# Performance work log

Measured on AMD Instinct MI355X. Metric: run time of the kernel, lower is better.

## Reference

```python
import jax, jax.numpy as jnp
import numpy as np

LN_EPS = 1e-5

def setup_inputs() -> dict:
    key = jax.random.key(0)
    ks = jax.random.split(key, 8)
    B, d, var_dim, hidden = 1024, 32, 64, 256
    in_dim = d * var_dim
    causal_vars = jax.random.normal(ks[0], (B, d, var_dim), dtype=jnp.float32)
    adj_soft = jax.random.uniform(ks[1], (d, d), dtype=jnp.float32)
    # Per-variable MLP params (stacked along leading d axis), torch-default-like init scale
    s1 = 1.0 / np.sqrt(in_dim)
    s2 = 1.0 / np.sqrt(hidden)
    W1 = jax.random.uniform(ks[2], (d, in_dim, hidden), minval=-s1, maxval=s1, dtype=jnp.float32)
    b1 = jax.random.uniform(ks[3], (d, hidden), minval=-s1, maxval=s1, dtype=jnp.float32)
    W2 = jax.random.uniform(ks[4], (d, hidden, var_dim), minval=-s2, maxval=s2, dtype=jnp.float32)
    b2 = jax.random.uniform(ks[5], (d, var_dim), minval=-s2, maxval=s2, dtype=jnp.float32)
    gamma = jnp.ones((d, var_dim), dtype=jnp.float32)
    beta = jnp.zeros((d, var_dim), dtype=jnp.float32)
    return {"causal_vars": causal_vars, "adj_soft": adj_soft, "W1": W1, "b1": b1,
            "W2": W2, "b2": b2, "gamma": gamma, "beta": beta}

def reference(causal_vars, adj_soft, W1, b1, W2, b2, gamma, beta):
    B, d, var_dim = causal_vars.shape
    # masked parent input for equation i: adj_soft[i, j] * causal_vars[b, j, :]
    # shape (B, d_eq, d_parent, var_dim) -> flatten parents: (B, d, d*var_dim)
    x = adj_soft[None, :, :, None] * causal_vars[:, None, :, :]
    x = x.reshape(B, d, d * var_dim)
    # grouped 2-layer MLP, distinct weights per variable i
    h = jnp.einsum('bik,ikh->bih', x, W1) + b1[None]
    h = jax.nn.gelu(h, approximate=False)
    y = jnp.einsum('bih,ihv->biv', h, W2) + b2[None]
    # LayerNorm over var_dim with per-variable affine params
    mu = jnp.mean(y, axis=-1, keepdims=True)
    var = jnp.var(y, axis=-1, keepdims=True)
    y = (y - mu) * jax.lax.rsqrt(var + LN_EPS)
    return y * gamma[None] + beta[None]  # (B, d, var_dim)
```

## Files before the change

kernel.cpp:

```cpp
#include <hip/hip_runtime.h>
#include <hip/hip_bf16.h>

typedef __bf16 bf16_t;
typedef __bf16 bf16x8 __attribute__((ext_vector_type(8)));
typedef float f32x4 __attribute__((ext_vector_type(4)));

#define NB 1024
#define ND 32
#define VD 64
#define NH 256
#define NK 2048

#define OFF_A    0
#define OFF_W1T  (4u*1024u*1024u)
#define OFF_W2T  (36u*1024u*1024u)

#define GLD16(gsrc, ldst) \
  __builtin_amdgcn_global_load_lds((const __attribute__((address_space(1))) void*)(gsrc), \
                                   (__attribute__((address_space(3))) void*)(ldst), 16, 0, 0)

__global__ __launch_bounds__(256) void prep_kernel(
    const float* __restrict__ cv, const float* __restrict__ adj,
    const float* __restrict__ W1, const float* __restrict__ W2,
    bf16_t* __restrict__ A, bf16_t* __restrict__ W1T, bf16_t* __restrict__ W2T)
{
  __shared__ float Ls[64 * 67];
  int bx = blockIdx.x;
  int tid = threadIdx.x;
  if (bx < 4096) {
    int i = bx >> 7;
    int rem = bx & 127;
    int k0 = (rem >> 2) * 64;
    int h0 = (rem & 3) * 64;
    float a = adj[i * 32 + (k0 >> 6)];
    int rrow = tid >> 4, c4 = (tid & 15) * 4;
#pragma unroll
    for (int p = 0; p < 4; ++p) {
      int row = p * 16 + rrow;
      const float* src = W1 + ((size_t)(i * 2048 + k0 + row)) * 256 + h0 + c4;
      float4 v = *(const float4*)src;
#pragma unroll
      for (int j = 0; j < 4; ++j) Ls[row * 67 + c4 + j] = a * ((const float*)&v)[j];
    }
    __syncthreads();
#pragma unroll
    for (int p = 0; p < 2; ++p) {
      int u = p * 256 + tid;
      int h = u >> 3, c8 = u & 7;
      bf16x8 o;
#pragma unroll
      for (int j = 0; j < 8; ++j) o[j] = (bf16_t)Ls[(c8 * 8 + j) * 67 + h];
      *(bf16x8*)(W1T + ((size_t)(i * 256 + h0 + h)) * 2048 + k0 + c8 * 8) = o;
    }
  } else if (bx < 5120) {
    int t = (bx - 4096) * 256 + tid;
    const float4* s = (const float4*)cv + (size_t)t * 2;
    float4 v0 = s[0], v1 = s[1];
    bf16x8 o;
    o[0] = (bf16_t)v0.x; o[1] = (bf16_t)v0.y; o[2] = (bf16_t)v0.z; o[3] = (bf16_t)v0.w;
    o[4] = (bf16_t)v1.x; o[5] = (bf16_t)v1.y; o[6] = (bf16_t)v1.z; o[7] = (bf16_t)v1.w;
    *(bf16x8*)(A + (size_t)t * 8) = o;
  } else {
    int t = (bx - 5120) * 256 + tid;
    int i = t >> 11;
    int rem = t & 2047;
    int h8 = rem >> 6;
    int v = rem & 63;
    const float* src = W2 + ((size_t)(i * 256 + h8 * 8)) * 64 + v;
    bf16x8 o;
#pragma unroll
    for (int r = 0; r < 8; ++r) o[r] = (bf16_t)src[(size_t)r * 64];
    *(bf16x8*)(W2T + ((size_t)(i * 64 + v)) * 256 + h8 * 8) = o;
  }
}

__global__ __launch_bounds__(512, 2) void sem_main_kernel(
    const bf16_t* __restrict__ A, const bf16_t* __restrict__ W1T,
    const bf16_t* __restrict__ W2T,
    const float* __restrict__ b1, const float* __restrict__ b2,
    const float* __restrict__ gamma, const float* __restrict__ beta,
    float* __restrict__ out)
{
  __shared__ char smem[98304];

  int p = blockIdx.x;
  int L = (p & 7) * 32 + (p >> 3);
  int i = L >> 3;
  int brow = (L & 7) * 128;

  int tid = threadIdx.x;
  int lane = tid & 63;
  int wid = tid >> 6;
  int wr = wid >> 2;
  int wc = wid & 3;
  int lhi = lane >> 4;
  int llo = lane & 15;

  f32x4 acc[4][4];
#pragma unroll
  for (int m = 0; m < 4; ++m)
#pragma unroll
    for (int n = 0; n < 4; ++n) acc[m][n] = (f32x4){0.f, 0.f, 0.f, 0.f};

  const bf16_t* W1Ti = W1T + (size_t)i * 256 * 2048;

  auto stage = [&](int b, int kt) {
    char* Ad = smem + b * 24576;
    char* Bd = Ad + 8192;
    {
      int row = tid >> 2, c = tid & 3;
      int sc = c ^ ((row >> 1) & 3);
      const bf16_t* g = A + (size_t)(brow + row) * 2048 + kt * 32 + sc * 8;
      GLD16(g, Ad + wid * 1024);
    }
#pragma unroll
    for (int it = 0; it < 2; ++it) {
      int s = tid + it * 512;
      int row = s >> 2, c = s & 3;
      int sc = c ^ ((row >> 1) & 3);
      const bf16_t* g = W1Ti + (size_t)row * 2048 + kt * 32 + sc * 8;
      GLD16(g, Bd + it * 8192 + wid * 1024);
    }
  };

  auto compute = [&](int t) {
    const char* At = smem + (t & 3) * 24576;
    const char* Bt = At + 8192;
    bf16x8 af[4], bfr[4];
#pragma unroll
    for (int m = 0; m < 4; ++m) {
      int row = wr * 64 + m * 16 + llo;
      int sc = lhi ^ ((row >> 1) & 3);
      af[m] = *(const bf16x8*)(At + row * 64 + sc * 16);
    }
#pragma unroll
    for (int n = 0; n < 4; ++n) {
      int hrow = wc * 64 + n * 16 + llo;
      int sc = lhi ^ ((hrow >> 1) & 3);
      bfr[n] = *(const bf16x8*)(Bt + hrow * 64 + sc * 16);
    }
    __builtin_amdgcn_s_setprio(1);
#pragma unroll
    for (int m = 0; m < 4; ++m)
#pragma unroll
      for (int n = 0; n < 4; ++n)
        acc[m][n] = __builtin_amdgcn_mfma_f32_16x16x32_bf16(af[m], bfr[n], acc[m][n], 0, 0, 0);
    __builtin_amdgcn_s_setprio(0);
  };

  asm volatile("" ::: "memory");
  stage(0, 0); stage(1, 1); stage(2, 2);

  for (int t = 0; t < 61; ++t) {
    asm volatile("s_waitcnt vmcnt(6)" ::: "memory");
    __builtin_amdgcn_s_barrier();
    asm volatile("" ::: "memory");
    stage((t + 3) & 3, t + 3);
    compute(t);
  }
  asm volatile("s_waitcnt vmcnt(6)" ::: "memory");
  __builtin_amdgcn_s_barrier();
  asm volatile("" ::: "memory");
  compute(61);
  asm volatile("s_waitcnt vmcnt(3)" ::: "memory");
  __builtin_amdgcn_s_barrier();
  asm volatile("" ::: "memory");
  compute(62);
  asm volatile("s_waitcnt vmcnt(0)" ::: "memory");
  __builtin_amdgcn_s_barrier();
  asm volatile("" ::: "memory");
  compute(63);

  __syncthreads();

  bf16_t* Hs = (bf16_t*)smem;
  float bias[4];
#pragma unroll
  for (int n = 0; n < 4; ++n) bias[n] = b1[i * 256 + wc * 64 + n * 16 + llo];
#pragma unroll
  for (int m = 0; m < 4; ++m) {
#pragma unroll
    for (int n = 0; n < 4; ++n) {
      int col = wc * 64 + n * 16 + llo;
#pragma unroll
      for (int r = 0; r < 4; ++r) {
        int row = wr * 64 + m * 16 + lhi * 4 + r;
        float x = acc[m][n][r] + bias[n];
        float gl = 0.5f * x * (1.0f + erff(x * 0.70710678118654752f));
        Hs[row * 264 + col] = (bf16_t)gl;
      }
    }
  }
  __syncthreads();

  f32x4 acc2[4];
#pragma unroll
  for (int n = 0; n < 4; ++n) acc2[n] = (f32x4){0.f, 0.f, 0.f, 0.f};
  const bf16_t* W2Ti = W2T + (size_t)i * 64 * 256;
#pragma unroll
  for (int kk = 0; kk < 8; ++kk) {
    int k = kk * 32 + lhi * 8;
    bf16x8 af = *(const bf16x8*)(Hs + (wid * 16 + llo) * 264 + k);
#pragma unroll
    for (int n = 0; n < 4; ++n) {
      bf16x8 bfr = *(const bf16x8*)(W2Ti + (size_t)(n * 16 + llo) * 256 + k);
      acc2[n] = __builtin_amdgcn_mfma_f32_16x16x32_bf16(af, bfr, acc2[n], 0, 0, 0);
    }
  }

  float b2v[4], gam[4], bet[4];
#pragma unroll
  for (int n = 0; n < 4; ++n) {
    int v = n * 16 + llo;
    b2v[n] = b2[i * 64 + v];
    gam[n] = gamma[i * 64 + v];
    bet[n] = beta[i * 64 + v];
  }
#pragma unroll
  for (int r = 0; r < 4; ++r) {
    float yv[4], s = 0.f, sq = 0.f;
#pragma unroll
    for (int n = 0; n < 4; ++n) {
      yv[n] = acc2[n][r] + b2v[n];
      s += yv[n];
      sq += yv[n] * yv[n];
    }
#pragma unroll
    for (int off = 1; off < 16; off <<= 1) {
      s += __shfl_xor(s, off, 64);
      sq += __shfl_xor(sq, off, 64);
    }
    float mu = s * (1.0f / 64.0f);
    float var = sq * (1.0f / 64.0f) - mu * mu;
    float rstd = rsqrtf(var + 1e-5f);
    int row = brow + wid * 16 + lhi * 4 + r;
    float* op = out + ((size_t)row * 32 + i) * 64;
#pragma unroll
    for (int n = 0; n < 4; ++n)
      op[n * 16 + llo] = (yv[n] - mu) * rstd * gam[n] + bet[n];
  }
}

extern "C" void kernel_launch(void* const* d_in, const int* in_sizes, int n_in,
                              void* d_out, int out_size, void* d_ws, size_t ws_size,
                              hipStream_t stream) {
  const float* cv    = (const float*)d_in[0];
  const float* adj   = (const float*)d_in[1];
  const float* W1    = (const float*)d_in[2];
  const float* b1    = (const float*)d_in[3];
  const float* W2    = (const float*)d_in[4];
  const float* b2    = (const float*)d_in[5];
  const float* gamma = (const float*)d_in[6];
  const float* beta  = (const float*)d_in[7];
  float* out = (float*)d_out;

  bf16_t* Abf  = (bf16_t*)((char*)d_ws + OFF_A);
  bf16_t* W1T  = (bf16_t*)((char*)d_ws + OFF_W1T);
  bf16_t* W2T  = (bf16_t*)((char*)d_ws + OFF_W2T);

  prep_kernel<<<5376, 256, 0, stream>>>(cv, adj, W1, W2, Abf, W1T, W2T);
  sem_main_kernel<<<256, 512, 0, stream>>>(Abf, W1T, W2T, b1, b2, gamma, beta, out);
}
```

Measured before the change: 68.82 us.

## Halve GEMM block tile to 64 rows with 256 threads and triple buffering

Shrinks the main kernel's block tile from 128×256 (8 waves) to 64×256 (4 waves), doubling the grid to 512 blocks so work spreads more evenly across CUs. The LDS pipeline drops from four stages to three, which cuts shared memory per block, and per-thread load and LDS offsets are now computed once outside the loop. In exchange, each W1 tile is fetched by twice as many blocks, which raises L2/HBM weight traffic and halves weight reuse per block.

```diff
diff --git a/kernel.cpp b/kernel.cpp
--- a/kernel.cpp
+++ b/kernel.cpp
@@ -74,71 +74,70 @@
   }
 }
 
-__global__ __launch_bounds__(512, 2) void sem_main_kernel(
+__global__ __launch_bounds__(256, 2) void sem_main_kernel(
     const bf16_t* __restrict__ A, const bf16_t* __restrict__ W1T,
     const bf16_t* __restrict__ W2T,
     const float* __restrict__ b1, const float* __restrict__ b2,
     const float* __restrict__ gamma, const float* __restrict__ beta,
     float* __restrict__ out)
 {
-  __shared__ char smem[98304];
+  __shared__ char smem[61440];
 
   int p = blockIdx.x;
-  int L = (p & 7) * 32 + (p >> 3);
-  int i = L >> 3;
-  int brow = (L & 7) * 128;
+  int L = (p & 7) * 64 + (p >> 3);
+  int i = L >> 4;
+  int brow = (L & 15) * 64;
 
   int tid = threadIdx.x;
   int lane = tid & 63;
   int wid = tid >> 6;
-  int wr = wid >> 2;
-  int wc = wid & 3;
   int lhi = lane >> 4;
   int llo = lane & 15;
 
+  const bf16_t* W1Ti = W1T + (size_t)i * 256 * 2048;
+
+  int arow = tid >> 2, ac = tid & 3;
+  const bf16_t* aSrc = A + (size_t)(brow + arow) * 2048 + (ac ^ ((arow >> 1) & 3)) * 8;
+  const bf16_t* bSrc0 = W1Ti + (size_t)arow * 2048 + (ac ^ ((arow >> 1) & 3)) * 8;
+  const bf16_t* bSrc1 = W1Ti + (size_t)(64 + arow) * 2048 + (ac ^ (((64 + arow) >> 1) & 3)) * 8;
+  const bf16_t* bSrc2 = W1Ti + (size_t)(128 + arow) * 2048 + (ac ^ (((128 + arow) >> 1) & 3)) * 8;
+  const bf16_t* bSrc3 = W1Ti + (size_t)(192 + arow) * 2048 + (ac ^ (((192 + arow) >> 1) & 3)) * 8;
+  int ldsW = wid * 1024;
+
+  auto stage = [&](int b, int kt) {
+    char* base = smem + b * 20480;
+    GLD16(aSrc + kt * 32, base + ldsW);
+    GLD16(bSrc0 + kt * 32, base + 4096 + ldsW);
+    GLD16(bSrc1 + kt * 32, base + 8192 + ldsW);
+    GLD16(bSrc2 + kt * 32, base + 12288 + ldsW);
+    GLD16(bSrc3 + kt * 32, base + 16384 + ldsW);
+  };
+
+  int aOff[4], bOff[4];
+#pragma unroll
+  for (int m = 0; m < 4; ++m) {
+    int row = m * 16 + llo;
+    aOff[m] = row * 64 + ((lhi ^ ((row >> 1) & 3)) * 16);
+  }
+#pragma unroll
+  for (int n = 0; n < 4; ++n) {
+    int row = wid * 64 + n * 16 + llo;
+    bOff[n] = 4096 + row * 64 + ((lhi ^ ((row >> 1) & 3)) * 16);
+  }
+
   f32x4 acc[4][4];
 #pragma unroll
   for (int m = 0; m < 4; ++m)
 #pragma unroll
     for (int n = 0; n < 4; ++n) acc[m][n] = (f32x4){0.f, 0.f, 0.f, 0.f};
 
-  const bf16_t* W1Ti = W1T + (size_t)i * 256 * 2048;
-
-  auto stage = [&](int b, int kt) {
-    char* Ad = smem + b * 24576;
-    char* Bd = Ad + 8192;
-    {
-      int row = tid >> 2, c = tid & 3;
-      int sc = c ^ ((row >> 1) & 3);
-      const bf16_t* g = A + (size_t)(brow + row) * 2048 + kt * 32 + sc * 8;
-      GLD16(g, Ad + wid * 1024);
-    }
-#pragma unroll
-    for (int it = 0; it < 2; ++it) {
-      int s = tid + it * 512;
-      int row = s >> 2, c = s & 3;
-      int sc = c ^ ((row >> 1) & 3);
-      const bf16_t* g = W1Ti + (size_t)row * 2048 + kt * 32 + sc * 8;
-      GLD16(g, Bd + it * 8192 + wid * 1024);
-    }
-  };
-
-  auto compute = [&](int t) {
-    const char* At = smem + (t & 3) * 24576;
-    const char* Bt = At + 8192;
+  auto compute = [&](int b) {
+    const char* base = smem + b * 20480;
     bf16x8 af[4], bfr[4];
 #pragma unroll
-    for (int m = 0; m < 4; ++m) {
-      int row = wr * 64 + m * 16 + llo;
-      int sc = lhi ^ ((row >> 1) & 3);
-      af[m] = *(const bf16x8*)(At + row * 64 + sc * 16);
-    }
-#pragma unroll
-    for (int n = 0; n < 4; ++n) {
-      int hrow = wc * 64 + n * 16 + llo;
-      int sc = lhi ^ ((hrow >> 1) & 3);
-      bfr[n] = *(const bf16x8*)(Bt + hrow * 64 + sc * 16);
-    }
+    for (int m = 0; m < 4; ++m) af[m] = *(const bf16x8*)(base + aOff[m]);
+#pragma unroll
+    for (int n = 0; n < 4; ++n) bfr[n] = *(const bf16x8*)(base + bOff[n]);
     __builtin_amdgcn_s_setprio(1);
 #pragma unroll
     for (int m = 0; m < 4; ++m)
@@ -149,42 +148,39 @@
   };
 
   asm volatile("" ::: "memory");
-  stage(0, 0); stage(1, 1); stage(2, 2);
-
-  for (int t = 0; t < 61; ++t) {
-    asm volatile("s_waitcnt vmcnt(6)" ::: "memory");
+  stage(0, 0); stage(1, 1);
+  int bc = 0, bs = 2;
+  for (int t = 0; t < 62; ++t) {
+    asm volatile("s_waitcnt vmcnt(5) lgkmcnt(0)" ::: "memory");
     __builtin_amdgcn_s_barrier();
     asm volatile("" ::: "memory");
-    stage((t + 3) & 3, t + 3);
-    compute(t);
-  }
-  asm volatile("s_waitcnt vmcnt(6)" ::: "memory");
+    stage(bs, t + 2);
+    compute(bc);
+    bc = (bc == 2) ? 0 : bc + 1;
+    bs = (bs == 2) ? 0 : bs + 1;
+  }
+  asm volatile("s_waitcnt vmcnt(5) lgkmcnt(0)" ::: "memory");
   __builtin_amdgcn_s_barrier();
   asm volatile("" ::: "memory");
-  compute(61);
-  asm volatile("s_waitcnt vmcnt(3)" ::: "memory");
+  compute(2);
+  asm volatile("s_waitcnt vmcnt(0) lgkmcnt(0)" ::: "memory");
   __builtin_amdgcn_s_barrier();
   asm volatile("" ::: "memory");
-  compute(62);
-  asm volatile("s_waitcnt vmcnt(0)" ::: "memory");
-  __builtin_amdgcn_s_barrier();
-  asm volatile("" ::: "memory");
-  compute(63);
-
+  compute(0);
   __syncthreads();
 
   bf16_t* Hs = (bf16_t*)smem;
   float bias[4];
 #pragma unroll
-  for (int n = 0; n < 4; ++n) bias[n] = b1[i * 256 + wc * 64 + n * 16 + llo];
+  for (int n = 0; n < 4; ++n) bias[n] = b1[i * 256 + wid * 64 + n * 16 + llo];
 #pragma unroll
   for (int m = 0; m < 4; ++m) {
 #pragma unroll
     for (int n = 0; n < 4; ++n) {
-      int col = wc * 64 + n * 16 + llo;
+      int col = wid * 64 + n * 16 + llo;
 #pragma unroll
       for (int r = 0; r < 4; ++r) {
-        int row = wr * 64 + m * 16 + lhi * 4 + r;
+        int row = m * 16 + lhi * 4 + r;
         float x = acc[m][n][r] + bias[n];
         float gl = 0.5f * x * (1.0f + erff(x * 0.70710678118654752f));
         Hs[row * 264 + col] = (bf16_t)gl;
@@ -259,5 +255,5 @@
   bf16_t* W2T  = (bf16_t*)((char*)d_ws + OFF_W2T);
 
   prep_kernel<<<5376, 256, 0, stream>>>(cv, adj, W1, W2, Abf, W1T, W2T);
-  sem_main_kernel<<<256, 512, 0, stream>>>(Abf, W1T, W2T, b1, b2, gamma, beta, out);
+  sem_main_kernel<<<512, 256, 0, stream>>>(Abf, W1T, W2T, b1, b2, gamma, beta, out);
 }
```

Measured after the change: 80.39 us. 1.17x slower.

## Restructure GEMM1 main loop into split-phase pipeline with interleaved LDS reads

Applied to the files above, without the earlier changes.

Replaces the 3-deep prefetch loop with a 2-ahead staged pipeline in which each k-tile is computed in two halves. LDS fragment reads for the second half are issued between barriers, so they overlap with the MFMAs of the first half. Global-to-LDS addresses and swizzled LDS offsets are precomputed outside the loop, and sched_barriers pin the instruction order. The cost is four barriers per k-tile instead of one and a shallower prefetch depth, which may expose more global latency.

```diff
diff --git a/kernel.cpp b/kernel.cpp
--- a/kernel.cpp
+++ b/kernel.cpp
@@ -74,6 +74,55 @@
   }
 }
 
+#define STAGE3(BUF, HT) do { \
+    char* _bb = smem + (BUF) * 24576; \
+    GLD16(aSrc  + (size_t)(HT) * 32, _bb + ldsA); \
+    GLD16(bSrc0 + (size_t)(HT) * 32, _bb + 8192  + ldsA); \
+    GLD16(bSrc1 + (size_t)(HT) * 32, _bb + 16384 + ldsA); \
+  } while (0)
+
+#define MFMA_COL(N, BFR) \
+  acc[0][N] = __builtin_amdgcn_mfma_f32_16x16x32_bf16(_af0, BFR, acc[0][N], 0, 0, 0); \
+  acc[1][N] = __builtin_amdgcn_mfma_f32_16x16x32_bf16(_af1, BFR, acc[1][N], 0, 0, 0); \
+  acc[2][N] = __builtin_amdgcn_mfma_f32_16x16x32_bf16(_af2, BFR, acc[2][N], 0, 0, 0); \
+  acc[3][N] = __builtin_amdgcn_mfma_f32_16x16x32_bf16(_af3, BFR, acc[3][N], 0, 0, 0);
+
+#define PHASE_PAIR(BUF, HT, DO_STAGE, VMASM) do { \
+    const char* _cb = smem + (BUF) * 24576; \
+    bf16x8 _af0 = *(const bf16x8*)(_cb + aOff0); \
+    bf16x8 _af1 = *(const bf16x8*)(_cb + aOff1); \
+    bf16x8 _af2 = *(const bf16x8*)(_cb + aOff2); \
+    bf16x8 _af3 = *(const bf16x8*)(_cb + aOff3); \
+    bf16x8 _bf0 = *(const bf16x8*)(_cb + bOff0); \
+    bf16x8 _bf1 = *(const bf16x8*)(_cb + bOff1); \
+    if (DO_STAGE) { STAGE3((BUF + 2) & 3, (HT) + 2); } \
+    asm volatile("" ::: "memory"); \
+    __builtin_amdgcn_s_barrier(); \
+    asm volatile("s_waitcnt lgkmcnt(0)" ::: "memory"); \
+    __builtin_amdgcn_sched_barrier(0); \
+    __builtin_amdgcn_s_setprio(1); \
+    MFMA_COL(0, _bf0) \
+    MFMA_COL(1, _bf1) \
+    __builtin_amdgcn_s_setprio(0); \
+    __builtin_amdgcn_sched_barrier(0); \
+    asm volatile("" ::: "memory"); \
+    __builtin_amdgcn_s_barrier(); \
+    bf16x8 _bf2 = *(const bf16x8*)(_cb + bOff2); \
+    bf16x8 _bf3 = *(const bf16x8*)(_cb + bOff3); \
+    asm volatile("" ::: "memory"); \
+    asm volatile(VMASM ::: "memory"); \
+    __builtin_amdgcn_s_barrier(); \
+    asm volatile("s_waitcnt lgkmcnt(0)" ::: "memory"); \
+    __builtin_amdgcn_sched_barrier(0); \
+    __builtin_amdgcn_s_setprio(1); \
+    MFMA_COL(2, _bf2) \
+    MFMA_COL(3, _bf3) \
+    __builtin_amdgcn_s_setprio(0); \
+    __builtin_amdgcn_sched_barrier(0); \
+    asm volatile("" ::: "memory"); \
+    __builtin_amdgcn_s_barrier(); \
+  } while (0)
+
 __global__ __launch_bounds__(512, 2) void sem_main_kernel(
     const bf16_t* __restrict__ A, const bf16_t* __restrict__ W1T,
     const bf16_t* __restrict__ W2T,
@@ -96,80 +145,48 @@
   int lhi = lane >> 4;
   int llo = lane & 15;
 
+  const bf16_t* W1Ti = W1T + (size_t)i * 256 * 2048;
+
+  int arow = tid >> 2, ac = tid & 3;
+  int sc0 = ac ^ ((arow >> 1) & 3);
+  const bf16_t* aSrc  = A + (size_t)(brow + arow) * 2048 + sc0 * 8;
+  const bf16_t* bSrc0 = W1Ti + (size_t)arow * 2048 + sc0 * 8;
+  const bf16_t* bSrc1 = W1Ti + (size_t)(128 + arow) * 2048 + sc0 * 8;
+  int ldsA = wid * 1024;
+
+  int ar0 = wr * 64 + 0 * 16 + llo, ar1 = wr * 64 + 16 + llo, ar2 = wr * 64 + 32 + llo, ar3 = wr * 64 + 48 + llo;
+  int aOff0 = ar0 * 64 + ((lhi ^ ((ar0 >> 1) & 3)) * 16);
+  int aOff1 = ar1 * 64 + ((lhi ^ ((ar1 >> 1) & 3)) * 16);
+  int aOff2 = ar2 * 64 + ((lhi ^ ((ar2 >> 1) & 3)) * 16);
+  int aOff3 = ar3 * 64 + ((lhi ^ ((ar3 >> 1) & 3)) * 16);
+  int br0 = wc * 64 + 0 * 16 + llo, br1 = wc * 64 + 16 + llo, br2 = wc * 64 + 32 + llo, br3 = wc * 64 + 48 + llo;
+  int bOff0 = 8192 + br0 * 64 + ((lhi ^ ((br0 >> 1) & 3)) * 16);
+  int bOff1 = 8192 + br1 * 64 + ((lhi ^ ((br1 >> 1) & 3)) * 16);
+  int bOff2 = 8192 + br2 * 64 + ((lhi ^ ((br2 >> 1) & 3)) * 16);
+  int bOff3 = 8192 + br3 * 64 + ((lhi ^ ((br3 >> 1) & 3)) * 16);
+
   f32x4 acc[4][4];
 #pragma unroll
   for (int m = 0; m < 4; ++m)
 #pragma unroll
     for (int n = 0; n < 4; ++n) acc[m][n] = (f32x4){0.f, 0.f, 0.f, 0.f};
 
-  const bf16_t* W1Ti = W1T + (size_t)i * 256 * 2048;
-
-  auto stage = [&](int b, int kt) {
-    char* Ad = smem + b * 24576;
-    char* Bd = Ad + 8192;
-    {
-      int row = tid >> 2, c = tid & 3;
-      int sc = c ^ ((row >> 1) & 3);
-      const bf16_t* g = A + (size_t)(brow + row) * 2048 + kt * 32 + sc * 8;
-      GLD16(g, Ad + wid * 1024);
-    }
-#pragma unroll
-    for (int it = 0; it < 2; ++it) {
-      int s = tid + it * 512;
-      int row = s >> 2, c = s & 3;
-      int sc = c ^ ((row >> 1) & 3);
-      const bf16_t* g = W1Ti + (size_t)row * 2048 + kt * 32 + sc * 8;
-      GLD16(g, Bd + it * 8192 + wid * 1024);
-    }
-  };
-
-  auto compute = [&](int t) {
-    const char* At = smem + (t & 3) * 24576;
-    const char* Bt = At + 8192;
-    bf16x8 af[4], bfr[4];
-#pragma unroll
-    for (int m = 0; m < 4; ++m) {
-      int row = wr * 64 + m * 16 + llo;
-      int sc = lhi ^ ((row >> 1) & 3);
-      af[m] = *(const bf16x8*)(At + row * 64 + sc * 16);
-    }
-#pragma unroll
-    for (int n = 0; n < 4; ++n) {
-      int hrow = wc * 64 + n * 16 + llo;
-      int sc = lhi ^ ((hrow >> 1) & 3);
-      bfr[n] = *(const bf16x8*)(Bt + hrow * 64 + sc * 16);
-    }
-    __builtin_amdgcn_s_setprio(1);
-#pragma unroll
-    for (int m = 0; m < 4; ++m)
-#pragma unroll
-      for (int n = 0; n < 4; ++n)
-        acc[m][n] = __builtin_amdgcn_mfma_f32_16x16x32_bf16(af[m], bfr[n], acc[m][n], 0, 0, 0);
-    __builtin_amdgcn_s_setprio(0);
-  };
-
   asm volatile("" ::: "memory");
-  stage(0, 0); stage(1, 1); stage(2, 2);
-
-  for (int t = 0; t < 61; ++t) {
-    asm volatile("s_waitcnt vmcnt(6)" ::: "memory");
-    __builtin_amdgcn_s_barrier();
-    asm volatile("" ::: "memory");
-    stage((t + 3) & 3, t + 3);
-    compute(t);
-  }
-  asm volatile("s_waitcnt vmcnt(6)" ::: "memory");
-  __builtin_amdgcn_s_barrier();
-  asm volatile("" ::: "memory");
-  compute(61);
+  STAGE3(0, 0);
+  STAGE3(1, 1);
   asm volatile("s_waitcnt vmcnt(3)" ::: "memory");
   __builtin_amdgcn_s_barrier();
-  asm volatile("" ::: "memory");
-  compute(62);
-  asm volatile("s_waitcnt vmcnt(0)" ::: "memory");
-  __builtin_amdgcn_s_barrier();
-  asm volatile("" ::: "memory");
-  compute(63);
+
+  for (int htb = 0; htb < 60; htb += 4) {
+    PHASE_PAIR(0, htb + 0, 1, "s_waitcnt vmcnt(3)");
+    PHASE_PAIR(1, htb + 1, 1, "s_waitcnt vmcnt(3)");
+    PHASE_PAIR(2, htb + 2, 1, "s_waitcnt vmcnt(3)");
+    PHASE_PAIR(3, htb + 3, 1, "s_waitcnt vmcnt(3)");
+  }
+  PHASE_PAIR(0, 60, 1, "s_waitcnt vmcnt(3)");
+  PHASE_PAIR(1, 61, 1, "s_waitcnt vmcnt(3)");
+  PHASE_PAIR(2, 62, 0, "s_waitcnt vmcnt(0)");
+  PHASE_PAIR(3, 63, 0, "");
 
   __syncthreads();
 
```

New measurement: 68.76 us. No clear change (-0.1%).
